# Optimization experiments

Measured on AMD Instinct MI355X. Metric: run time of the kernel, lower is better.

## Reference

```python
import jax, jax.numpy as jnp
import numpy as np

B, T, M, D, DOUT = 2, 10000, 100000, 128, 128


def setup_inputs() -> dict:
    key = jax.random.key(0)
    k1, k2, k3, k4, k5, k6 = jax.random.split(key, 6)
    x_1st = jax.random.normal(k1, (B, T, 2, D), dtype=jnp.float32)
    x_2nd = jax.random.normal(k2, (B, M, 4, D), dtype=jnp.float32)  # unused in forward math
    edge = jax.random.randint(k3, (2, M), 0, T, dtype=jnp.int32)
    A_masked = jax.random.normal(k4, (B, 1, M), dtype=jnp.float32)
    W = jax.random.normal(k5, (DOUT, D), dtype=jnp.float32) / jnp.sqrt(jnp.float32(D))
    b = jax.random.normal(k6, (DOUT,), dtype=jnp.float32) * 0.01
    return {"x_1st": x_1st, "x_2nd": x_2nd, "edge": edge, "A_masked": A_masked, "W": W, "b": b}


def reference(x_1st, x_2nd, edge, A_masked, W, b):
    node_in, node_out = edge[0], edge[1]  # (M,)
    w = A_masked[:, 0, :, None]  # (B, M, 1) edge weights

    def node_message_passing(x):  # x: (B, T, d)
        msg = x[:, node_out, :] * w                        # gather + edge-weight mul: (B, M, d)
        upd = jnp.zeros_like(x).at[:, node_in, :].add(msg)  # scatter_add into T nodes
        return x + upd

    x_neg = node_message_passing(x_1st[:, :, 0, :])
    x_pos = node_message_passing(x_1st[:, :, 1, :])
    x = jnp.stack([x_neg, x_pos], axis=2)  # (B, T, 2, d)
    return jnp.einsum("btcd,od->btco", x, W) + b  # node_layer Linear
```

## Files before the change

kernel.cpp:

```cpp
#include <hip/hip_runtime.h>
#include <hip/hip_bf16.h>

#define BB    2
#define TT    10000
#define MM    100000
#define DD    128
#define DOUTN 128
#define NROWS (BB * TT * 2)
#define NTILES (NROWS / 16)
#define WPITCH 136

typedef float  f32x4  __attribute__((ext_vector_type(4)));
typedef short  bf16x8 __attribute__((ext_vector_type(8)));

static __device__ __forceinline__ short f2bf(float f) {
    union { float f; unsigned u; } v; v.f = f;
    unsigned r = v.u + 0x7fffu + ((v.u >> 16) & 1u);
    return (short)(r >> 16);
}

__global__ __launch_bounds__(256)
void gemm_y_kernel(const float* __restrict__ X, const float* __restrict__ W,
                   float* __restrict__ y) {
    __shared__ __align__(16) short Wb[DOUTN * WPITCH];

    const int tid = threadIdx.x;
    {
        const int n  = tid >> 1;
        const int kh = (tid & 1) * 64;
        const float* wp = W + n * DD + kh;
        short* dst = &Wb[n * WPITCH + kh];
#pragma unroll
        for (int e = 0; e < 8; ++e) {
            float4 a = *(const float4*)(wp + e * 8);
            float4 b = *(const float4*)(wp + e * 8 + 4);
            bf16x8 t;
            t[0] = f2bf(a.x); t[1] = f2bf(a.y); t[2] = f2bf(a.z); t[3] = f2bf(a.w);
            t[4] = f2bf(b.x); t[5] = f2bf(b.y); t[6] = f2bf(b.z); t[7] = f2bf(b.w);
            *(bf16x8*)(dst + e * 8) = t;
        }
    }
    __syncthreads();

    const int lane = tid & 63;
    const int wid  = tid >> 6;
    const int l15  = lane & 15;
    const int q    = lane >> 4;
    const int tile = blockIdx.x * 4 + wid;

    bf16x8 bfrag[8][4];
#pragma unroll
    for (int ot = 0; ot < 8; ++ot)
#pragma unroll
        for (int s = 0; s < 4; ++s)
            bfrag[ot][s] = *(const bf16x8*)&Wb[(ot * 16 + l15) * WPITCH + s * 32 + q * 8];

    const float* xp = X + (size_t)(tile * 16 + l15) * DD + q * 8;
    bf16x8 afrag[4];
#pragma unroll
    for (int s = 0; s < 4; ++s) {
        float4 a0 = *(const float4*)(xp + s * 32);
        float4 a1 = *(const float4*)(xp + s * 32 + 4);
        bf16x8 t;
        t[0] = f2bf(a0.x); t[1] = f2bf(a0.y); t[2] = f2bf(a0.z); t[3] = f2bf(a0.w);
        t[4] = f2bf(a1.x); t[5] = f2bf(a1.y); t[6] = f2bf(a1.z); t[7] = f2bf(a1.w);
        afrag[s] = t;
    }

    f32x4 acc[8];
#pragma unroll
    for (int ot = 0; ot < 8; ++ot) acc[ot] = (f32x4){0.f, 0.f, 0.f, 0.f};
#pragma unroll
    for (int s = 0; s < 4; ++s)
#pragma unroll
        for (int ot = 0; ot < 8; ++ot)
            acc[ot] = __builtin_amdgcn_mfma_f32_16x16x32_bf16(afrag[s], bfrag[ot][s], acc[ot], 0, 0, 0);

#pragma unroll
    for (int ot = 0; ot < 8; ++ot) {
        const int col = ot * 16 + l15;
#pragma unroll
        for (int r = 0; r < 4; ++r) {
            const int row = tile * 16 + q * 4 + r;
            y[(size_t)row * DOUTN + col] = acc[ot][r];
        }
    }
}

__global__ __launch_bounds__(256)
void hist_kernel(const int* __restrict__ edge, int* __restrict__ cnt) {
    const int m = blockIdx.x * 256 + threadIdx.x;
    if (m < MM) atomicAdd(&cnt[edge[m]], 1);
}

#define SCAN_T 1024
#define SCAN_CH 10
__global__ __launch_bounds__(SCAN_T)
void scan_kernel(int* __restrict__ cur) {
    __shared__ int sh[SCAN_T];
    const int tid = threadIdx.x;
    int vals[SCAN_CH];
    int sum = 0;
    const int base_i = tid * SCAN_CH;
#pragma unroll
    for (int j = 0; j < SCAN_CH; ++j) {
        const int i = base_i + j;
        const int v = (i < TT) ? cur[i] : 0;
        vals[j] = v; sum += v;
    }
    sh[tid] = sum;
    __syncthreads();
    for (int off = 1; off < SCAN_T; off <<= 1) {
        const int v = (tid >= off) ? sh[tid - off] : 0;
        __syncthreads();
        sh[tid] += v;
        __syncthreads();
    }
    int run = (tid == 0) ? 0 : sh[tid - 1];
#pragma unroll
    for (int j = 0; j < SCAN_CH; ++j) {
        const int i = base_i + j;
        if (i < TT) { cur[i] = run; run += vals[j]; }
    }
}

__global__ __launch_bounds__(256)
void fill_kernel(const int* __restrict__ edge, int* __restrict__ cur,
                 int* __restrict__ bucket) {
    const int m = blockIdx.x * 256 + threadIdx.x;
    if (m < MM) {
        const int p = atomicAdd(&cur[edge[m]], 1);
        bucket[p] = m;
    }
}

__global__ __launch_bounds__(256)
void gather_kernel(const float* __restrict__ y, const int* __restrict__ edge,
                   const float* __restrict__ Am, const int* __restrict__ cur_end,
                   const int* __restrict__ bucket, const float* __restrict__ bias,
                   float* __restrict__ out) {
    const int lane = threadIdx.x & 63;
    const int t    = blockIdx.x * 4 + (threadIdx.x >> 6);

    const int end   = cur_end[t];
    const int start = (t == 0) ? 0 : cur_end[t - 1];

    const float* yb0 = y + (size_t)t * 256;
    const float* yb1 = y + (size_t)(TT + t) * 256;
    float2 a00 = ((const float2*)yb0)[lane];
    float2 a01 = ((const float2*)(yb0 + 128))[lane];
    float2 a10 = ((const float2*)yb1)[lane];
    float2 a11 = ((const float2*)(yb1 + 128))[lane];

    const int* esrc = edge + MM;

    for (int base = start; base < end; base += 64) {
        const int n = min(end - base, 64);
        int nout = 0; float w0 = 0.f, w1 = 0.f;
        if (lane < n) {
            const int m = bucket[base + lane];
            nout = esrc[m];
            w0   = Am[m];
            w1   = Am[MM + m];
        }
        for (int e = 0; e < n; ++e) {
            const int   no  = __builtin_amdgcn_readlane(nout, e);
            const float ww0 = __uint_as_float(__builtin_amdgcn_readlane(__float_as_uint(w0), e));
            const float ww1 = __uint_as_float(__builtin_amdgcn_readlane(__float_as_uint(w1), e));
            const float* p0 = y + (size_t)no * 256;
            const float* p1 = y + (size_t)(TT + no) * 256;
            const float2 v00 = ((const float2*)p0)[lane];
            const float2 v01 = ((const float2*)(p0 + 128))[lane];
            const float2 v10 = ((const float2*)p1)[lane];
            const float2 v11 = ((const float2*)(p1 + 128))[lane];
            a00.x += ww0 * v00.x; a00.y += ww0 * v00.y;
            a01.x += ww0 * v01.x; a01.y += ww0 * v01.y;
            a10.x += ww1 * v10.x; a10.y += ww1 * v10.y;
            a11.x += ww1 * v11.x; a11.y += ww1 * v11.y;
        }
    }

    const float2 bs = ((const float2*)bias)[lane];
    float* o0 = out + (size_t)t * 256;
    float* o1 = out + (size_t)(TT + t) * 256;
    float2 r;
    r.x = a00.x + bs.x; r.y = a00.y + bs.y; ((float2*)o0)[lane]         = r;
    r.x = a01.x + bs.x; r.y = a01.y + bs.y; ((float2*)(o0 + 128))[lane] = r;
    r.x = a10.x + bs.x; r.y = a10.y + bs.y; ((float2*)o1)[lane]         = r;
    r.x = a11.x + bs.x; r.y = a11.y + bs.y; ((float2*)(o1 + 128))[lane] = r;
}

extern "C" void kernel_launch(void* const* d_in, const int* in_sizes, int n_in,
                              void* d_out, int out_size, void* d_ws, size_t ws_size,
                              hipStream_t stream) {
    const float* x1   = (const float*)d_in[0];
    const int*   edge = (const int*)d_in[2];
    const float* Am   = (const float*)d_in[3];
    const float* W    = (const float*)d_in[4];
    const float* bias = (const float*)d_in[5];
    float* out = (float*)d_out;

    float* y      = (float*)d_ws;
    int*   cur    = (int*)d_ws + (size_t)NROWS * DOUTN;
    int*   bucket = cur + TT;

    hipMemsetAsync(cur, 0, TT * sizeof(int), stream);
    hist_kernel<<<(MM + 255) / 256, 256, 0, stream>>>(edge, cur);
    scan_kernel<<<1, SCAN_T, 0, stream>>>(cur);
    fill_kernel<<<(MM + 255) / 256, 256, 0, stream>>>(edge, cur, bucket);

    gemm_y_kernel<<<NTILES / 4, 256, 0, stream>>>(x1, W, y);

    gather_kernel<<<TT / 4, 256, 0, stream>>>(y, edge, Am, cur, bucket, bias, out);
}
```

Measured before the change: 524.1 us.

## Fuse CSR build into one persistent kernel with grid barriers; unroll gather by two

Folds the histogram, scan and bucket-fill kernels into a single persistent kernel of 256 blocks that uses software grid barriers built on atomic counters. This removes two kernel launches and their serialization gaps. The gather loop is also unrolled by two so each wave keeps more independent row loads in flight. The software barrier relies on all 256 blocks being co-resident, which is safe on a large GPU but adds spin-wait cost, and the scan now runs in one block while the other blocks idle.

```diff
diff --git a/kernel.cpp b/kernel.cpp
--- a/kernel.cpp
+++ b/kernel.cpp
@@ -9,6 +9,7 @@
 #define NROWS (BB * TT * 2)
 #define NTILES (NROWS / 16)
 #define WPITCH 136
+#define CSR_NB 256
 
 typedef float  f32x4  __attribute__((ext_vector_type(4)));
 typedef short  bf16x8 __attribute__((ext_vector_type(8)));
@@ -87,48 +88,62 @@
     }
 }
 
-__global__ __launch_bounds__(256)
-void hist_kernel(const int* __restrict__ edge, int* __restrict__ cnt) {
-    const int m = blockIdx.x * 256 + threadIdx.x;
-    if (m < MM) atomicAdd(&cnt[edge[m]], 1);
-}
-
-#define SCAN_T 1024
-#define SCAN_CH 10
-__global__ __launch_bounds__(SCAN_T)
-void scan_kernel(int* __restrict__ cur) {
-    __shared__ int sh[SCAN_T];
+static __device__ __forceinline__ void grid_bar(int* c, int nb) {
+    __syncthreads();
+    if (threadIdx.x == 0) {
+        __threadfence();
+        atomicAdd(c, 1);
+        while (__hip_atomic_load(c, __ATOMIC_ACQUIRE, __HIP_MEMORY_SCOPE_AGENT) < nb) {
+            __builtin_amdgcn_s_sleep(8);
+        }
+    }
+    __syncthreads();
+}
+
+__global__ __launch_bounds__(256, 2)
+void csr_kernel(const int* __restrict__ edge, int* __restrict__ cur,
+                int* __restrict__ bucket, int* __restrict__ bar) {
     const int tid = threadIdx.x;
-    int vals[SCAN_CH];
-    int sum = 0;
-    const int base_i = tid * SCAN_CH;
-#pragma unroll
-    for (int j = 0; j < SCAN_CH; ++j) {
-        const int i = base_i + j;
-        const int v = (i < TT) ? cur[i] : 0;
-        vals[j] = v; sum += v;
-    }
-    sh[tid] = sum;
-    __syncthreads();
-    for (int off = 1; off < SCAN_T; off <<= 1) {
-        const int v = (tid >= off) ? sh[tid - off] : 0;
+
+    for (int m = blockIdx.x * 256 + tid; m < MM; m += 256 * CSR_NB)
+        atomicAdd(&cur[edge[m]], 1);
+
+    grid_bar(&bar[0], CSR_NB);
+
+    if (blockIdx.x == 0) {
+        __shared__ int sh[256];
+        int vals[40];
+        int sum = 0;
+        const int base_i = tid * 40;
+#pragma unroll
+        for (int j = 0; j < 40; ++j) {
+            const int i = base_i + j;
+            const int v = (i < TT)
+                ? __hip_atomic_load(&cur[i], __ATOMIC_RELAXED, __HIP_MEMORY_SCOPE_AGENT) : 0;
+            vals[j] = v; sum += v;
+        }
+        sh[tid] = sum;
         __syncthreads();
-        sh[tid] += v;
-        __syncthreads();
-    }
-    int run = (tid == 0) ? 0 : sh[tid - 1];
-#pragma unroll
-    for (int j = 0; j < SCAN_CH; ++j) {
-        const int i = base_i + j;
-        if (i < TT) { cur[i] = run; run += vals[j]; }
-    }
-}
-
-__global__ __launch_bounds__(256)
-void fill_kernel(const int* __restrict__ edge, int* __restrict__ cur,
-                 int* __restrict__ bucket) {
-    const int m = blockIdx.x * 256 + threadIdx.x;
-    if (m < MM) {
+        for (int off = 1; off < 256; off <<= 1) {
+            const int v = (tid >= off) ? sh[tid - off] : 0;
+            __syncthreads();
+            sh[tid] += v;
+            __syncthreads();
+        }
+        int run = (tid == 0) ? 0 : sh[tid - 1];
+#pragma unroll
+        for (int j = 0; j < 40; ++j) {
+            const int i = base_i + j;
+            if (i < TT) {
+                __hip_atomic_store(&cur[i], run, __ATOMIC_RELAXED, __HIP_MEMORY_SCOPE_AGENT);
+                run += vals[j];
+            }
+        }
+    }
+
+    grid_bar(&bar[1], CSR_NB);
+
+    for (int m = blockIdx.x * 256 + tid; m < MM; m += 256 * CSR_NB) {
         const int p = atomicAdd(&cur[edge[m]], 1);
         bucket[p] = m;
     }
@@ -163,7 +178,36 @@
             w0   = Am[m];
             w1   = Am[MM + m];
         }
-        for (int e = 0; e < n; ++e) {
+        int e = 0;
+        for (; e + 2 <= n; e += 2) {
+            const int   noA = __builtin_amdgcn_readlane(nout, e);
+            const float wA0 = __uint_as_float(__builtin_amdgcn_readlane(__float_as_uint(w0), e));
+            const float wA1 = __uint_as_float(__builtin_amdgcn_readlane(__float_as_uint(w1), e));
+            const int   noB = __builtin_amdgcn_readlane(nout, e + 1);
+            const float wB0 = __uint_as_float(__builtin_amdgcn_readlane(__float_as_uint(w0), e + 1));
+            const float wB1 = __uint_as_float(__builtin_amdgcn_readlane(__float_as_uint(w1), e + 1));
+            const float* pA0 = y + (size_t)noA * 256;
+            const float* pA1 = y + (size_t)(TT + noA) * 256;
+            const float* pB0 = y + (size_t)noB * 256;
+            const float* pB1 = y + (size_t)(TT + noB) * 256;
+            const float2 vA00 = ((const float2*)pA0)[lane];
+            const float2 vA01 = ((const float2*)(pA0 + 128))[lane];
+            const float2 vA10 = ((const float2*)pA1)[lane];
+            const float2 vA11 = ((const float2*)(pA1 + 128))[lane];
+            const float2 vB00 = ((const float2*)pB0)[lane];
+            const float2 vB01 = ((const float2*)(pB0 + 128))[lane];
+            const float2 vB10 = ((const float2*)pB1)[lane];
+            const float2 vB11 = ((const float2*)(pB1 + 128))[lane];
+            a00.x += wA0 * vA00.x; a00.y += wA0 * vA00.y;
+            a01.x += wA0 * vA01.x; a01.y += wA0 * vA01.y;
+            a10.x += wA1 * vA10.x; a10.y += wA1 * vA10.y;
+            a11.x += wA1 * vA11.x; a11.y += wA1 * vA11.y;
+            a00.x += wB0 * vB00.x; a00.y += wB0 * vB00.y;
+            a01.x += wB0 * vB01.x; a01.y += wB0 * vB01.y;
+            a10.x += wB1 * vB10.x; a10.y += wB1 * vB10.y;
+            a11.x += wB1 * vB11.x; a11.y += wB1 * vB11.y;
+        }
+        if (e < n) {
             const int   no  = __builtin_amdgcn_readlane(nout, e);
             const float ww0 = __uint_as_float(__builtin_amdgcn_readlane(__float_as_uint(w0), e));
             const float ww1 = __uint_as_float(__builtin_amdgcn_readlane(__float_as_uint(w1), e));
@@ -202,14 +246,11 @@
 
     float* y      = (float*)d_ws;
     int*   cur    = (int*)d_ws + (size_t)NROWS * DOUTN;
-    int*   bucket = cur + TT;
-
-    hipMemsetAsync(cur, 0, TT * sizeof(int), stream);
-    hist_kernel<<<(MM + 255) / 256, 256, 0, stream>>>(edge, cur);
-    scan_kernel<<<1, SCAN_T, 0, stream>>>(cur);
-    fill_kernel<<<(MM + 255) / 256, 256, 0, stream>>>(edge, cur, bucket);
-
+    int*   bar    = cur + TT;
+    int*   bucket = bar + 8;
+
+    hipMemsetAsync(cur, 0, (TT + 8) * sizeof(int), stream);
+    csr_kernel<<<CSR_NB, 256, 0, stream>>>(edge, cur, bucket, bar);
     gemm_y_kernel<<<NTILES / 4, 256, 0, stream>>>(x1, W, y);
-
     gather_kernel<<<TT / 4, 256, 0, stream>>>(y, edge, Am, cur, bucket, bias, out);
 }
```

Measured after the change: 699.5 us. 33.5% more time.
